# Kernel tuning notes

Measured on AMD Instinct MI355X. Metric: run time of the kernel, lower is better.

## Reference

```python
import jax, jax.numpy as jnp
import numpy as np

# RReLU in eval mode == LeakyReLU with slope (lower+upper)/2, defaults 1/8, 1/3
RRELU_SLOPE = (1.0 / 8.0 + 1.0 / 3.0) / 2.0


def rrelu(x):
    return jnp.where(x >= 0, x, x * RRELU_SLOPE)


def _linear_params(key, fan_in, fan_out):
    kw, kb = jax.random.split(key)
    s = 1.0 / np.sqrt(fan_in)
    W = jax.random.uniform(kw, (fan_in, fan_out), minval=-s, maxval=s, dtype=jnp.float32)
    b = jax.random.uniform(kb, (fan_out,), minval=-s, maxval=s, dtype=jnp.float32)
    return W, b


def setup_inputs() -> dict:
    key = jax.random.key(0)
    ks = jax.random.split(key, 6)
    B, L, D_TS, D_SEQ, HID = 64, 2048, 8, 120, 64
    DIN = D_TS + D_SEQ
    ts = jax.random.normal(ks[0], (B, L, D_TS), dtype=jnp.float32)
    seq = jax.random.normal(ks[1], (B, L, D_SEQ), dtype=jnp.float32)
    lengths = jax.random.randint(ks[2], (B,), 1, L + 1, dtype=jnp.int32)
    Wk, bk = _linear_params(ks[3], DIN, HID)
    Wq, bq = _linear_params(ks[4], DIN, HID)
    Wv, bv = _linear_params(ks[5], DIN, HID)
    return {"ts": ts, "seq": seq, "lengths": lengths,
            "Wk": Wk, "bk": bk, "Wq": Wq, "bq": bq, "Wv": Wv, "bv": bv}


def reference(ts, seq, lengths, Wk, bk, Wq, bq, Wv, bv):
    # packed_cat([ts, seq]) -> concat along feature dim; padded positions masked later
    x = jnp.concatenate([ts, seq], axis=-1)              # [B, L, Din]
    k = rrelu(jnp.einsum('bld,dh->blh', x, Wk) + bk)     # [B, L, H]
    v = rrelu(jnp.einsum('bld,dh->blh', x, Wv) + bv)     # [B, L, H]
    q = rrelu(jnp.einsum('bld,dh->blh', x, Wq) + bq)     # [B, L, H]
    B, L, _ = x.shape
    # get_last_vectors_unpadded: last valid token of each sequence
    q_last = q[jnp.arange(B), lengths - 1]               # [B, H]
    scores = jnp.einsum('bh,blh->bl', q_last, k)         # [B, L]
    valid = jnp.arange(L)[None, :] < lengths[:, None]    # [B, L]
    scores = jnp.where(valid, scores, -jnp.inf)
    attn = jax.nn.softmax(scores, axis=-1)               # masked softmax over seq
    return jnp.einsum('bl,blh->bh', attn, v)             # [B, H]
```

## Files before the change

kernel.cpp:

```cpp
#include <hip/hip_runtime.h>
#include <hip/hip_bf16.h>

#define B_   64
#define L_   2048
#define DTS  8
#define DSEQ 120
#define H_   64
#define TILE 64
#define NT   32

typedef unsigned short u16;
typedef unsigned int   u32;
typedef __bf16 bf16x8 __attribute__((ext_vector_type(8)));
typedef short  short8 __attribute__((ext_vector_type(8)));
typedef float  f32x4  __attribute__((ext_vector_type(4)));

__device__ __forceinline__ float rrelu_f(float x) {
    return x >= 0.f ? x : x * 0.22916666666666666f;
}
__device__ __forceinline__ u16 f2bf(float x) {
    unsigned u = __float_as_uint(x);
    return (u16)((u + 0x7FFFu + ((u >> 16) & 1u)) >> 16);
}
__device__ __forceinline__ float bf2f(u16 u) {
    return __uint_as_float(((unsigned)u) << 16);
}
__device__ __forceinline__ void dma16(void* lds, const void* g) {
    __builtin_amdgcn_global_load_lds(
        (const __attribute__((address_space(1))) unsigned*)g,
        (__attribute__((address_space(3))) unsigned*)lds, 16, 0, 0);
}

__global__ void setup_kernel(const float* __restrict__ ts, const float* __restrict__ seq,
                             const int* __restrict__ lengths,
                             const float* __restrict__ Wk, const float* __restrict__ Wv,
                             const float* __restrict__ Wq, const float* __restrict__ bq,
                             u16* __restrict__ packw, float* __restrict__ qlast)
{
    const int blk = blockIdx.x, tid = threadIdx.x;
    if (blk < 64) {
        const int f = blk * 256 + tid;
        const int idx = f & 8191;
        const bool isK = f < 8192;
        const float* W = isK ? Wk : Wv;
        u16* hi = packw + (isK ? 0 : 16384);
        u16* lo = hi + 8192;
        const int j = idx & 7, lane = (idx >> 3) & 63, kk = (idx >> 9) & 3, ni = idx >> 11;
        const int kd = kk * 32 + (lane >> 4) * 8 + j;
        const int n  = ni * 16 + (lane & 15);
        const float v = W[kd * H_ + n];
        const u16 h = f2bf(v);
        hi[idx] = h;
        lo[idx] = f2bf(v - bf2f(h));
    } else {
        const int b = blk - 64;
        const int h = tid & 63, part = tid >> 6;
        const int l = lengths[b] - 1;
        const float* tsr = ts  + ((size_t)b * L_ + l) * DTS;
        const float* sqr = seq + ((size_t)b * L_ + l) * DSEQ;
        float acc = 0.f;
        if (part == 0) {
            #pragma unroll
            for (int d = 0; d < DTS; ++d)  acc += tsr[d] * Wq[d * H_ + h];
            #pragma unroll
            for (int d = DTS; d < 32; ++d) acc += sqr[d - DTS] * Wq[d * H_ + h];
        } else {
            const int d0 = part * 32;
            #pragma unroll
            for (int i = 0; i < 32; ++i)
                acc += sqr[d0 + i - DTS] * Wq[(d0 + i) * H_ + h];
        }
        __shared__ float qred[4][H_];
        qred[part][h] = acc;
        __syncthreads();
        if (tid < H_)
            qlast[b * H_ + tid] = rrelu_f(qred[0][tid] + qred[1][tid] +
                                          qred[2][tid] + qred[3][tid] + bq[tid]);
    }
}

__global__ __launch_bounds__(512) void tile_kernel(
    const float* __restrict__ ts, const float* __restrict__ seq,
    const int* __restrict__ lengths,
    const u16* __restrict__ packw,
    const float* __restrict__ bk, const float* __restrict__ bv,
    const float* __restrict__ qlast,
    float* __restrict__ pden, float* __restrict__ pnum)
{
    const int b = blockIdx.y, t = blockIdx.x;
    const int len = lengths[b];
    const int ls = t * TILE;
    if (ls >= len) return;
    const int nv = min(TILE, len - ls);
    const int pb = b * NT + t;

    const int tid = threadIdx.x, wave = tid >> 6, lane = tid & 63;
    const int quad = lane >> 4, l16 = lane & 15;
    const int w4 = wave & 3, isV = wave >> 2;
    const int m0 = w4 * 16;

    __shared__ __align__(16) float xs[TILE * 128];
    __shared__ float scp[TILE];
    __shared__ float red[4][H_];
    __shared__ float wd[4];

    const float* bts = ts  + (size_t)(b * L_ + ls) * DTS;
    const float* bsq = seq + (size_t)(b * L_ + ls) * DSEQ;
    #pragma unroll
    for (int i = 0; i < 4; ++i) {
        const int CI = wave * 256 + i * 64 + lane;
        const int row = CI >> 5, cp = CI & 31;
        const int c = cp ^ (row & 7);
        char* dst = (char*)xs + (size_t)(wave * 256 + i * 64) * 16;
        if (c < 2) dma16(dst, bts + (size_t)row * DTS  + c * 4);
        else       dma16(dst, bsq + (size_t)row * DSEQ + (c - 2) * 4);
    }

    const u16* bhp = packw + (isV ? 16384 : 0);
    const u16* blp = bhp + 8192;
    const float* bias = isV ? bv : bk;
    float bb[4], qv[4];
    #pragma unroll
    for (int ni = 0; ni < 4; ++ni) {
        bb[ni] = bias[ni * 16 + l16];
        qv[ni] = qlast[b * H_ + ni * 16 + l16];
    }
    __syncthreads();

    bf16x8 ah[4], al[4];
    {
        const int row = m0 + l16;
        const float* rb = xs + row * 128;
        const int sw = row & 7;
        #pragma unroll
        for (int kk = 0; kk < 4; ++kk) {
            const int c0 = kk * 8 + quad * 2;
            const f32x4 u = *(const f32x4*)(rb + ((c0 ^ sw) * 4));
            const f32x4 w = *(const f32x4*)(rb + (((c0 + 1) ^ sw) * 4));
            short8 h8, l8;
            #pragma unroll
            for (int j = 0; j < 4; ++j) {
                const u16 h0 = f2bf(u[j]);
                h8[j] = (short)h0; l8[j] = (short)f2bf(u[j] - bf2f(h0));
                const u16 h1 = f2bf(w[j]);
                h8[4 + j] = (short)h1; l8[4 + j] = (short)f2bf(w[j] - bf2f(h1));
            }
            ah[kk] = __builtin_bit_cast(bf16x8, h8);
            al[kk] = __builtin_bit_cast(bf16x8, l8);
        }
    }

    float cd[4][4];
    #pragma unroll
    for (int ni = 0; ni < 4; ++ni) {
        f32x4 acc = {0.f, 0.f, 0.f, 0.f};
        #pragma unroll
        for (int kk = 0; kk < 4; ++kk) {
            const size_t off = (size_t)((ni * 4 + kk) * 64 + lane) * 8;
            const bf16x8 bh = *(const bf16x8*)(bhp + off);
            const bf16x8 bl = *(const bf16x8*)(blp + off);
            acc = __builtin_amdgcn_mfma_f32_16x16x32_bf16(ah[kk], bh, acc, 0, 0, 0);
            acc = __builtin_amdgcn_mfma_f32_16x16x32_bf16(al[kk], bh, acc, 0, 0, 0);
            acc = __builtin_amdgcn_mfma_f32_16x16x32_bf16(ah[kk], bl, acc, 0, 0, 0);
        }
        #pragma unroll
        for (int r = 0; r < 4; ++r) cd[ni][r] = rrelu_f(acc[r] + bb[ni]);
    }

    if (!isV) {
        float ps[4] = {0.f, 0.f, 0.f, 0.f};
        #pragma unroll
        for (int ni = 0; ni < 4; ++ni)
            #pragma unroll
            for (int r = 0; r < 4; ++r) ps[r] += qv[ni] * cd[ni][r];
        #pragma unroll
        for (int mk = 1; mk < 16; mk <<= 1)
            #pragma unroll
            for (int r = 0; r < 4; ++r) ps[r] += __shfl_xor(ps[r], mk);
        float p4[4], ds = 0.f;
        #pragma unroll
        for (int r = 0; r < 4; ++r) {
            const int rr = m0 + quad * 4 + r;
            p4[r] = (rr < nv) ? __expf(fminf(ps[r], 80.f)) : 0.f;
            ds += p4[r];
        }
        if (l16 == 0) {
            #pragma unroll
            for (int r = 0; r < 4; ++r) scp[m0 + quad * 4 + r] = p4[r];
        }
        ds += __shfl_xor(ds, 16);
        ds += __shfl_xor(ds, 32);
        if (lane == 0) wd[w4] = ds;
    }
    __syncthreads();

    if (isV) {
        float pr[4];
        #pragma unroll
        for (int r = 0; r < 4; ++r) pr[r] = scp[m0 + quad * 4 + r];
        float pv[4];
        #pragma unroll
        for (int ni = 0; ni < 4; ++ni) {
            float a = 0.f;
            #pragma unroll
            for (int r = 0; r < 4; ++r) a += pr[r] * cd[ni][r];
            pv[ni] = a;
        }
        #pragma unroll
        for (int mk = 16; mk < 64; mk <<= 1)
            #pragma unroll
            for (int ni = 0; ni < 4; ++ni) pv[ni] += __shfl_xor(pv[ni], mk);
        if (quad == 0) {
            #pragma unroll
            for (int ni = 0; ni < 4; ++ni) red[w4][ni * 16 + l16] = pv[ni];
        }
    }
    __syncthreads();

    if (tid < H_)
        pnum[(size_t)pb * H_ + tid] = red[0][tid] + red[1][tid] + red[2][tid] + red[3][tid];
    if (tid == 0)
        pden[pb] = wd[0] + wd[1] + wd[2] + wd[3];
}

__global__ void combine_kernel(const int* __restrict__ lengths,
                               const float* __restrict__ pden,
                               const float* __restrict__ pnum,
                               float* __restrict__ out)
{
    const int b = blockIdx.x, h = threadIdx.x;
    const int nt = (lengths[b] + TILE - 1) / TILE;
    float den = 0.f, num = 0.f;
    #pragma unroll 8
    for (int t = 0; t < nt; ++t) {
        den += pden[b * NT + t];
        num += pnum[(size_t)(b * NT + t) * H_ + h];
    }
    out[b * H_ + h] = num / den;
}

extern "C" void kernel_launch(void* const* d_in, const int* in_sizes, int n_in,
                              void* d_out, int out_size, void* d_ws, size_t ws_size,
                              hipStream_t stream)
{
    const float* ts      = (const float*)d_in[0];
    const float* seq     = (const float*)d_in[1];
    const int*   lengths = (const int*)d_in[2];
    const float* Wk      = (const float*)d_in[3];
    const float* bk      = (const float*)d_in[4];
    const float* Wq      = (const float*)d_in[5];
    const float* bq      = (const float*)d_in[6];
    const float* Wv      = (const float*)d_in[7];
    const float* bv      = (const float*)d_in[8];

    float* ws    = (float*)d_ws;
    float* qlast = ws;
    float* pden  = ws + 4096;
    float* pnum  = ws + 6144;
    u16*   packw = (u16*)(ws + 137216);

    setup_kernel<<<dim3(128), dim3(256), 0, stream>>>(ts, seq, lengths, Wk, Wv, Wq, bq,
                                                      packw, qlast);
    tile_kernel<<<dim3(NT, B_), dim3(512), 0, stream>>>(ts, seq, lengths, packw,
                                                        bk, bv, qlast, pden, pnum);
    combine_kernel<<<dim3(B_), dim3(H_), 0, stream>>>(lengths, pden, pnum, (float*)d_out);
}
```

Before: 129.4 us.

## Fuse setup, tile and combine into one cooperative persistent kernel with double-buffered tiles

Merges the three launches into a single cooperative kernel with 256 persistent blocks that use grid-wide syncs between the phases. Each block handles up to 8 tiles, pairing tile T with tile 31-T across four batches to balance variable sequence lengths. The next tile is prefetched by DMA into a second LDS buffer while the current one is computed. This removes the gaps between kernel launches and evens out the load, at the cost of grid.sync overhead, a doubled LDS footprint that can lower occupancy, and reduced parallelism, since only 256 blocks run instead of up to 2048.

```diff
diff --git a/kernel.cpp b/kernel.cpp
--- a/kernel.cpp
+++ b/kernel.cpp
@@ -1,5 +1,8 @@
 #include <hip/hip_runtime.h>
 #include <hip/hip_bf16.h>
+#include <hip/hip_cooperative_groups.h>
+
+namespace cg = cooperative_groups;
 
 #define B_   64
 #define L_   2048
@@ -8,6 +11,8 @@
 #define H_   64
 #define TILE 64
 #define NT   32
+#define NBLK 256
+#define TPB  8
 
 typedef unsigned short u16;
 typedef unsigned int   u32;
@@ -31,212 +36,228 @@
         (__attribute__((address_space(3))) unsigned*)lds, 16, 0, 0);
 }
 
-__global__ void setup_kernel(const float* __restrict__ ts, const float* __restrict__ seq,
-                             const int* __restrict__ lengths,
-                             const float* __restrict__ Wk, const float* __restrict__ Wv,
-                             const float* __restrict__ Wq, const float* __restrict__ bq,
-                             u16* __restrict__ packw, float* __restrict__ qlast)
+__global__ __launch_bounds__(512) void fused_kernel(
+    const float* __restrict__ ts, const float* __restrict__ seq,
+    const int* __restrict__ lengths,
+    const float* __restrict__ Wk, const float* __restrict__ bk,
+    const float* __restrict__ Wq, const float* __restrict__ bq,
+    const float* __restrict__ Wv, const float* __restrict__ bv,
+    u16* __restrict__ packw, float* __restrict__ qlast,
+    float* __restrict__ pden, float* __restrict__ pnum,
+    float* __restrict__ out)
 {
+    cg::grid_group grid = cg::this_grid();
     const int blk = blockIdx.x, tid = threadIdx.x;
+    const int wave = tid >> 6, lane = tid & 63;
+    const int quad = lane >> 4, l16 = lane & 15;
+
+    __shared__ __align__(16) float xs[2][TILE * 128];
+    __shared__ float scp[TILE];
+    __shared__ float red[4][H_];
+    __shared__ float wd[4];
+
     if (blk < 64) {
-        const int f = blk * 256 + tid;
+        const int b = blk, part = wave, h = lane;
+        const int l = lengths[b] - 1;
+        const float* tsr = ts  + ((size_t)b * L_ + l) * DTS;
+        const float* sqr = seq + ((size_t)b * L_ + l) * DSEQ;
+        float acc = 0.f;
+        const int d0 = part * 16;
+        #pragma unroll
+        for (int i = 0; i < 16; ++i) {
+            const int d = d0 + i;
+            const float xv = (d < DTS) ? tsr[d] : sqr[d - DTS];
+            acc += xv * Wq[d * H_ + h];
+        }
+        float* qr = (float*)xs;
+        qr[part * H_ + h] = acc;
+        __syncthreads();
+        if (tid < H_) {
+            float s = bq[tid];
+            #pragma unroll
+            for (int p = 0; p < 8; ++p) s += qr[p * H_ + tid];
+            qlast[b * H_ + tid] = rrelu_f(s);
+        }
+    } else if (blk < 96) {
+        const int f = (blk - 64) * 512 + tid;
+        const bool isK = f < 8192;
         const int idx = f & 8191;
-        const bool isK = f < 8192;
         const float* W = isK ? Wk : Wv;
         u16* hi = packw + (isK ? 0 : 16384);
         u16* lo = hi + 8192;
-        const int j = idx & 7, lane = (idx >> 3) & 63, kk = (idx >> 9) & 3, ni = idx >> 11;
-        const int kd = kk * 32 + (lane >> 4) * 8 + j;
-        const int n  = ni * 16 + (lane & 15);
+        const int j = idx & 7, ln = (idx >> 3) & 63, kk = (idx >> 9) & 3, ni = idx >> 11;
+        const int kd = kk * 32 + (ln >> 4) * 8 + j;
+        const int n  = ni * 16 + (ln & 15);
         const float v = W[kd * H_ + n];
         const u16 h = f2bf(v);
         hi[idx] = h;
         lo[idx] = f2bf(v - bf2f(h));
-    } else {
-        const int b = blk - 64;
-        const int h = tid & 63, part = tid >> 6;
-        const int l = lengths[b] - 1;
-        const float* tsr = ts  + ((size_t)b * L_ + l) * DTS;
-        const float* sqr = seq + ((size_t)b * L_ + l) * DSEQ;
-        float acc = 0.f;
-        if (part == 0) {
+    }
+    grid.sync();
+
+    const int w4 = wave & 3, isV = wave >> 2, m0 = w4 * 16;
+    const int T = blk >> 4;
+    const int bb0 = (blk & 15) * 4;
+    int len4[4];
+    #pragma unroll
+    for (int i = 0; i < 4; ++i) len4[i] = lengths[bb0 + i];
+
+    #define SLOT_B(i) (bb0 + ((i) & 3))
+    #define SLOT_T(i) (((i) < 4) ? T : (31 - T))
+    #define SLOT_VALID(i) (SLOT_T(i) * TILE < len4[(i) & 3])
+
+    int cur = 0;
+    while (cur < TPB && !SLOT_VALID(cur)) ++cur;
+
+    if (cur < TPB) {
+        auto issue = [&](int b, int t, int buf) {
+            const float* bts = ts  + (size_t)(b * L_ + t * TILE) * DTS;
+            const float* bsq = seq + (size_t)(b * L_ + t * TILE) * DSEQ;
             #pragma unroll
-            for (int d = 0; d < DTS; ++d)  acc += tsr[d] * Wq[d * H_ + h];
+            for (int i = 0; i < 4; ++i) {
+                const int CI = wave * 256 + i * 64 + lane;
+                const int row = CI >> 5, cp = CI & 31;
+                const int c = cp ^ (row & 7);
+                char* dst = (char*)&xs[buf][0] + (size_t)(wave * 256 + i * 64) * 16;
+                if (c < 2) dma16(dst, bts + (size_t)row * DTS  + c * 4);
+                else       dma16(dst, bsq + (size_t)row * DSEQ + (c - 2) * 4);
+            }
+        };
+
+        int buf = 0;
+        issue(SLOT_B(cur), SLOT_T(cur), buf);
+        while (cur < TPB) {
+            int nn = cur + 1;
+            while (nn < TPB && !SLOT_VALID(nn)) ++nn;
+            const int b = SLOT_B(cur), t = SLOT_T(cur);
+            const int nv = min(TILE, len4[cur & 3] - t * TILE);
+            const int pb = b * NT + t;
+
+            __syncthreads();
+            if (nn < TPB) issue(SLOT_B(nn), SLOT_T(nn), buf ^ 1);
+
+            bf16x8 ah[4], al[4];
+            {
+                const int row = m0 + l16;
+                const float* rb = &xs[buf][0] + row * 128;
+                const int sw = row & 7;
+                #pragma unroll
+                for (int kk = 0; kk < 4; ++kk) {
+                    const int c0 = kk * 8 + quad * 2;
+                    const f32x4 u = *(const f32x4*)(rb + ((c0 ^ sw) * 4));
+                    const f32x4 w = *(const f32x4*)(rb + (((c0 + 1) ^ sw) * 4));
+                    short8 h8, l8;
+                    #pragma unroll
+                    for (int j = 0; j < 4; ++j) {
+                        const u16 h0 = f2bf(u[j]);
+                        h8[j] = (short)h0; l8[j] = (short)f2bf(u[j] - bf2f(h0));
+                        const u16 h1 = f2bf(w[j]);
+                        h8[4 + j] = (short)h1; l8[4 + j] = (short)f2bf(w[j] - bf2f(h1));
+                    }
+                    ah[kk] = __builtin_bit_cast(bf16x8, h8);
+                    al[kk] = __builtin_bit_cast(bf16x8, l8);
+                }
+            }
+
+            const u16* bhp = packw + (isV ? 16384 : 0);
+            const u16* blp = bhp + 8192;
+            const float* bias = isV ? bv : bk;
+
+            float cd[4][4];
             #pragma unroll
-            for (int d = DTS; d < 32; ++d) acc += sqr[d - DTS] * Wq[d * H_ + h];
-        } else {
-            const int d0 = part * 32;
-            #pragma unroll
-            for (int i = 0; i < 32; ++i)
-                acc += sqr[d0 + i - DTS] * Wq[(d0 + i) * H_ + h];
-        }
-        __shared__ float qred[4][H_];
-        qred[part][h] = acc;
-        __syncthreads();
-        if (tid < H_)
-            qlast[b * H_ + tid] = rrelu_f(qred[0][tid] + qred[1][tid] +
-                                          qred[2][tid] + qred[3][tid] + bq[tid]);
+            for (int ni = 0; ni < 4; ++ni) {
+                f32x4 acc = {0.f, 0.f, 0.f, 0.f};
+                #pragma unroll
+                for (int kk = 0; kk < 4; ++kk) {
+                    const size_t off = (size_t)((ni * 4 + kk) * 64 + lane) * 8;
+                    const bf16x8 bh = *(const bf16x8*)(bhp + off);
+                    const bf16x8 bl = *(const bf16x8*)(blp + off);
+                    acc = __builtin_amdgcn_mfma_f32_16x16x32_bf16(ah[kk], bh, acc, 0, 0, 0);
+                    acc = __builtin_amdgcn_mfma_f32_16x16x32_bf16(al[kk], bh, acc, 0, 0, 0);
+                    acc = __builtin_amdgcn_mfma_f32_16x16x32_bf16(ah[kk], bl, acc, 0, 0, 0);
+                }
+                #pragma unroll
+                for (int r = 0; r < 4; ++r)
+                    cd[ni][r] = rrelu_f(acc[r] + bias[ni * 16 + l16]);
+            }
+
+            if (!isV) {
+                float ps[4] = {0.f, 0.f, 0.f, 0.f};
+                #pragma unroll
+                for (int ni = 0; ni < 4; ++ni) {
+                    const float qv = qlast[b * H_ + ni * 16 + l16];
+                    #pragma unroll
+                    for (int r = 0; r < 4; ++r) ps[r] += qv * cd[ni][r];
+                }
+                #pragma unroll
+                for (int mk = 1; mk < 16; mk <<= 1)
+                    #pragma unroll
+                    for (int r = 0; r < 4; ++r) ps[r] += __shfl_xor(ps[r], mk);
+                float p4[4], ds = 0.f;
+                #pragma unroll
+                for (int r = 0; r < 4; ++r) {
+                    const int rr = m0 + quad * 4 + r;
+                    p4[r] = (rr < nv) ? __expf(fminf(ps[r], 80.f)) : 0.f;
+                    ds += p4[r];
+                }
+                if (l16 == 0) {
+                    #pragma unroll
+                    for (int r = 0; r < 4; ++r) scp[m0 + quad * 4 + r] = p4[r];
+                }
+                ds += __shfl_xor(ds, 16);
+                ds += __shfl_xor(ds, 32);
+                if (lane == 0) wd[w4] = ds;
+            }
+            __syncthreads();
+
+            if (isV) {
+                float pr[4];
+                #pragma unroll
+                for (int r = 0; r < 4; ++r) pr[r] = scp[m0 + quad * 4 + r];
+                float pv[4];
+                #pragma unroll
+                for (int ni = 0; ni < 4; ++ni) {
+                    float a = 0.f;
+                    #pragma unroll
+                    for (int r = 0; r < 4; ++r) a += pr[r] * cd[ni][r];
+                    pv[ni] = a;
+                }
+                #pragma unroll
+                for (int mk = 16; mk < 64; mk <<= 1)
+                    #pragma unroll
+                    for (int ni = 0; ni < 4; ++ni) pv[ni] += __shfl_xor(pv[ni], mk);
+                if (quad == 0) {
+                    #pragma unroll
+                    for (int ni = 0; ni < 4; ++ni) red[w4][ni * 16 + l16] = pv[ni];
+                }
+            }
+            __syncthreads();
+
+            if (tid < H_)
+                pnum[(size_t)pb * H_ + tid] =
+                    red[0][tid] + red[1][tid] + red[2][tid] + red[3][tid];
+            if (tid == 0)
+                pden[pb] = wd[0] + wd[1] + wd[2] + wd[3];
+
+            cur = nn;
+            buf ^= 1;
+        }
     }
-}
-
-__global__ __launch_bounds__(512) void tile_kernel(
-    const float* __restrict__ ts, const float* __restrict__ seq,
-    const int* __restrict__ lengths,
-    const u16* __restrict__ packw,
-    const float* __restrict__ bk, const float* __restrict__ bv,
-    const float* __restrict__ qlast,
-    float* __restrict__ pden, float* __restrict__ pnum)
-{
-    const int b = blockIdx.y, t = blockIdx.x;
-    const int len = lengths[b];
-    const int ls = t * TILE;
-    if (ls >= len) return;
-    const int nv = min(TILE, len - ls);
-    const int pb = b * NT + t;
-
-    const int tid = threadIdx.x, wave = tid >> 6, lane = tid & 63;
-    const int quad = lane >> 4, l16 = lane & 15;
-    const int w4 = wave & 3, isV = wave >> 2;
-    const int m0 = w4 * 16;
-
-    __shared__ __align__(16) float xs[TILE * 128];
-    __shared__ float scp[TILE];
-    __shared__ float red[4][H_];
-    __shared__ float wd[4];
-
-    const float* bts = ts  + (size_t)(b * L_ + ls) * DTS;
-    const float* bsq = seq + (size_t)(b * L_ + ls) * DSEQ;
-    #pragma unroll
-    for (int i = 0; i < 4; ++i) {
-        const int CI = wave * 256 + i * 64 + lane;
-        const int row = CI >> 5, cp = CI & 31;
-        const int c = cp ^ (row & 7);
-        char* dst = (char*)xs + (size_t)(wave * 256 + i * 64) * 16;
-        if (c < 2) dma16(dst, bts + (size_t)row * DTS  + c * 4);
-        else       dma16(dst, bsq + (size_t)row * DSEQ + (c - 2) * 4);
+    grid.sync();
+
+    if (blk < 64 && tid < H_) {
+        const int b = blk;
+        const int nt = (lengths[b] + TILE - 1) / TILE;
+        float den = 0.f, num = 0.f;
+        for (int t = 0; t < nt; ++t) {
+            den += pden[b * NT + t];
+            num += pnum[(size_t)(b * NT + t) * H_ + tid];
+        }
+        out[b * H_ + tid] = num / den;
     }
-
-    const u16* bhp = packw + (isV ? 16384 : 0);
-    const u16* blp = bhp + 8192;
-    const float* bias = isV ? bv : bk;
-    float bb[4], qv[4];
-    #pragma unroll
-    for (int ni = 0; ni < 4; ++ni) {
-        bb[ni] = bias[ni * 16 + l16];
-        qv[ni] = qlast[b * H_ + ni * 16 + l16];
-    }
-    __syncthreads();
-
-    bf16x8 ah[4], al[4];
-    {
-        const int row = m0 + l16;
-        const float* rb = xs + row * 128;
-        const int sw = row & 7;
-        #pragma unroll
-        for (int kk = 0; kk < 4; ++kk) {
-            const int c0 = kk * 8 + quad * 2;
-            const f32x4 u = *(const f32x4*)(rb + ((c0 ^ sw) * 4));
-            const f32x4 w = *(const f32x4*)(rb + (((c0 + 1) ^ sw) * 4));
-            short8 h8, l8;
-            #pragma unroll
-            for (int j = 0; j < 4; ++j) {
-                const u16 h0 = f2bf(u[j]);
-                h8[j] = (short)h0; l8[j] = (short)f2bf(u[j] - bf2f(h0));
-                const u16 h1 = f2bf(w[j]);
-                h8[4 + j] = (short)h1; l8[4 + j] = (short)f2bf(w[j] - bf2f(h1));
-            }
-            ah[kk] = __builtin_bit_cast(bf16x8, h8);
-            al[kk] = __builtin_bit_cast(bf16x8, l8);
-        }
-    }
-
-    float cd[4][4];
-    #pragma unroll
-    for (int ni = 0; ni < 4; ++ni) {
-        f32x4 acc = {0.f, 0.f, 0.f, 0.f};
-        #pragma unroll
-        for (int kk = 0; kk < 4; ++kk) {
-            const size_t off = (size_t)((ni * 4 + kk) * 64 + lane) * 8;
-            const bf16x8 bh = *(const bf16x8*)(bhp + off);
-            const bf16x8 bl = *(const bf16x8*)(blp + off);
-            acc = __builtin_amdgcn_mfma_f32_16x16x32_bf16(ah[kk], bh, acc, 0, 0, 0);
-            acc = __builtin_amdgcn_mfma_f32_16x16x32_bf16(al[kk], bh, acc, 0, 0, 0);
-            acc = __builtin_amdgcn_mfma_f32_16x16x32_bf16(ah[kk], bl, acc, 0, 0, 0);
-        }
-        #pragma unroll
-        for (int r = 0; r < 4; ++r) cd[ni][r] = rrelu_f(acc[r] + bb[ni]);
-    }
-
-    if (!isV) {
-        float ps[4] = {0.f, 0.f, 0.f, 0.f};
-        #pragma unroll
-        for (int ni = 0; ni < 4; ++ni)
-            #pragma unroll
-            for (int r = 0; r < 4; ++r) ps[r] += qv[ni] * cd[ni][r];
-        #pragma unroll
-        for (int mk = 1; mk < 16; mk <<= 1)
-            #pragma unroll
-            for (int r = 0; r < 4; ++r) ps[r] += __shfl_xor(ps[r], mk);
-        float p4[4], ds = 0.f;
-        #pragma unroll
-        for (int r = 0; r < 4; ++r) {
-            const int rr = m0 + quad * 4 + r;
-            p4[r] = (rr < nv) ? __expf(fminf(ps[r], 80.f)) : 0.f;
-            ds += p4[r];
-        }
-        if (l16 == 0) {
-            #pragma unroll
-            for (int r = 0; r < 4; ++r) scp[m0 + quad * 4 + r] = p4[r];
-        }
-        ds += __shfl_xor(ds, 16);
-        ds += __shfl_xor(ds, 32);
-        if (lane == 0) wd[w4] = ds;
-    }
-    __syncthreads();
-
-    if (isV) {
-        float pr[4];
-        #pragma unroll
-        for (int r = 0; r < 4; ++r) pr[r] = scp[m0 + quad * 4 + r];
-        float pv[4];
-        #pragma unroll
-        for (int ni = 0; ni < 4; ++ni) {
-            float a = 0.f;
-            #pragma unroll
-            for (int r = 0; r < 4; ++r) a += pr[r] * cd[ni][r];
-            pv[ni] = a;
-        }
-        #pragma unroll
-        for (int mk = 16; mk < 64; mk <<= 1)
-            #pragma unroll
-            for (int ni = 0; ni < 4; ++ni) pv[ni] += __shfl_xor(pv[ni], mk);
-        if (quad == 0) {
-            #pragma unroll
-            for (int ni = 0; ni < 4; ++ni) red[w4][ni * 16 + l16] = pv[ni];
-        }
-    }
-    __syncthreads();
-
-    if (tid < H_)
-        pnum[(size_t)pb * H_ + tid] = red[0][tid] + red[1][tid] + red[2][tid] + red[3][tid];
-    if (tid == 0)
-        pden[pb] = wd[0] + wd[1] + wd[2] + wd[3];
-}
-
-__global__ void combine_kernel(const int* __restrict__ lengths,
-                               const float* __restrict__ pden,
-                               const float* __restrict__ pnum,
-                               float* __restrict__ out)
-{
-    const int b = blockIdx.x, h = threadIdx.x;
-    const int nt = (lengths[b] + TILE - 1) / TILE;
-    float den = 0.f, num = 0.f;
-    #pragma unroll 8
-    for (int t = 0; t < nt; ++t) {
-        den += pden[b * NT + t];
-        num += pnum[(size_t)(b * NT + t) * H_ + h];
-    }
-    out[b * H_ + h] = num / den;
+    #undef SLOT_B
+    #undef SLOT_T
+    #undef SLOT_VALID
 }
 
 extern "C" void kernel_launch(void* const* d_in, const int* in_sizes, int n_in,
@@ -258,10 +279,13 @@
     float* pden  = ws + 4096;
     float* pnum  = ws + 6144;
     u16*   packw = (u16*)(ws + 137216);
-
-    setup_kernel<<<dim3(128), dim3(256), 0, stream>>>(ts, seq, lengths, Wk, Wv, Wq, bq,
-                                                      packw, qlast);
-    tile_kernel<<<dim3(NT, B_), dim3(512), 0, stream>>>(ts, seq, lengths, packw,
-                                                        bk, bv, qlast, pden, pnum);
-    combine_kernel<<<dim3(B_), dim3(H_), 0, stream>>>(lengths, pden, pnum, (float*)d_out);
-}
+    float* outp  = (float*)d_out;
+
+    void* params[] = {
+        (void*)&ts, (void*)&seq, (void*)&lengths,
+        (void*)&Wk, (void*)&bk, (void*)&Wq, (void*)&bq, (void*)&Wv, (void*)&bv,
+        (void*)&packw, (void*)&qlast, (void*)&pden, (void*)&pnum, (void*)&outp
+    };
+    hipLaunchCooperativeKernel((const void*)fused_kernel, dim3(NBLK), dim3(512),
+                               params, 0, stream);
+}
```

After: 208.8 us. 1.61x slower.
